# Kernel optimization log

Hardware: AMD Instinct MI355X
Metric: run time of the kernel (lower is better)

## Reference

```python
import jax, jax.numpy as jnp
import numpy as np

N_NODES = 200_000
BRANCH = 8      # n: one-hot width / max children encoded
K_DEPTH = 16    # k: number of stacked levels, h_emb = n*k


def setup_inputs() -> dict:
    b, N = BRANCH, N_NODES
    idx = np.arange(N, dtype=np.int64)
    # complete b-ary forest (single tree): parent of node i is (i-1)//b
    parent = np.maximum((idx - 1) // b, 0)
    child_idx = np.where(idx > 0, (idx - 1) % b, 0)
    # depth via level start offsets of a complete b-ary tree
    starts = np.array([(b ** d - 1) // (b - 1) for d in range(K_DEPTH + 1)], dtype=np.int64)
    depth = (np.searchsorted(starts, idx, side='right') - 1).astype(np.int32)
    # p_emb buffer: p**i with p = 1.0 (unused by the original forward)
    p_emb = jnp.ones((BRANCH * K_DEPTH,), dtype=jnp.float32)
    return {
        'parent': jnp.asarray(parent, jnp.int32),
        'child_idx': jnp.asarray(child_idx, jnp.int32),
        'depth': jnp.asarray(depth, jnp.int32),
        'p_emb': p_emb,
        'n': BRANCH,
        'k': K_DEPTH,
    }


def reference(parent, child_idx, depth, p_emb, n, k):
    """Level-parallel tree positional embedding.

    Original per-node loop: child.pos[n:] = parent.pos[:-n]; child.pos[:n] = eye_row.
    Equivalent top-down level sweep: at level d, every node takes its parent's
    embedding shifted right by n slots and prepends the one-hot of its sibling
    index (one_hot yields zeros for child_idx >= n, matching torch.eye rows).
    """
    N = parent.shape[0]
    h = n * k
    onehot = jax.nn.one_hot(child_idx, n, dtype=jnp.float32)  # [N, n]

    def body(d, emb):
        par = emb[parent]                                      # [N, h] gather
        shifted = jnp.concatenate([onehot, par[:, : h - n]], axis=1)
        return jnp.where((depth == d)[:, None], shifted, emb)

    emb0 = jnp.zeros((N, h), dtype=jnp.float32)                # roots stay zero
    pos_embeds = jax.lax.fori_loop(1, k + 1, body, emb0)
    return pos_embeds
```

## Files before the change

### kernel.cpp

```cpp
#include <hip/hip_runtime.h>


#define PE_K 16
#define ROWS_PER_BLOCK 128

typedef float vf4 __attribute__((ext_vector_type(4)));

__global__ __launch_bounds__(256) void PositionalEmbedding_kernel(
    const int* __restrict__ parent,
    const int* __restrict__ child_idx,
    const int* __restrict__ depth,
    float* __restrict__ out,
    int N) {
  __shared__ unsigned long long codes[ROWS_PER_BLOCK];

  const int tid  = threadIdx.x;
  const int row0 = blockIdx.x * ROWS_PER_BLOCK;

  if (tid < ROWS_PER_BLOCK) {
    int row = row0 + tid;
    unsigned long long code = 0;
    if (row < N) {
      int d  = depth[row];
      int dd = d < PE_K ? d : PE_K;
      int cur = row;
      for (int j = 0; j < dd; ++j) {
        int ci = child_idx[cur] & 7;
        code |= (unsigned long long)ci << (3 * j);
        cur = parent[cur];
      }
      code |= (unsigned long long)dd << 48;
    }
    codes[tid] = code;
  }
  __syncthreads();

  const int c  = tid & 31;
  const int g  = tid >> 5;
  const int j  = c >> 1;
  const int sh = 3 * j;
  const int r0 = 4 * c - 8 * j;

  vf4* p = reinterpret_cast<vf4*>(out) + ((long long)(row0 + g) * 32 + c);
  const int last_full_rl = N - row0;

  #pragma unroll
  for (int it = 0; it < ROWS_PER_BLOCK / 8; ++it) {
    int rl = it * 8 + g;
    unsigned long long code = codes[rl];
    int dd = (int)(code >> 48);
    int ci = (int)((code >> sh) & 7);
    ci = (j < dd) ? ci : 8;

    vf4 v;
    v.x = (ci == r0 + 0) ? 1.f : 0.f;
    v.y = (ci == r0 + 1) ? 1.f : 0.f;
    v.z = (ci == r0 + 2) ? 1.f : 0.f;
    v.w = (ci == r0 + 3) ? 1.f : 0.f;

    if (rl < last_full_rl) __builtin_nontemporal_store(v, p);
    p += 8 * 32;
  }
}

extern "C" void kernel_launch(void* const* d_in, const int* in_sizes, int n_in,
                              void* d_out, int out_size, void* d_ws, size_t ws_size,
                              hipStream_t stream) {
  const int* parent    = (const int*)d_in[0];
  const int* child_idx = (const int*)d_in[1];
  const int* depth     = (const int*)d_in[2];
  float* out = (float*)d_out;
  int N = in_sizes[0];

  int grid = (N + ROWS_PER_BLOCK - 1) / ROWS_PER_BLOCK;
  PositionalEmbedding_kernel<<<grid, 256, 0, stream>>>(parent, child_idx, depth, out, N);
}
```

Before: 25.78 us.

## Split tree walk and one-hot expansion into two kernels via workspace

Splits the fused kernel in two. The first kernel walks each node's ancestor chain and packs the sibling indices into 4-bit nibbles, writing one 64-bit code per node to the workspace; 8 is the sentinel for an empty slot. The second kernel expands these codes into the output with one float4 per thread across the whole grid, which removes the 128-row serial walk at block granularity and the shared-memory barrier. This adds a second launch and an extra global round-trip for the codes. It also replaces nontemporal stores with plain stores in the expand path and in the fallback fused kernel.

```diff
diff --git a/kernel.cpp b/kernel.cpp
--- a/kernel.cpp
+++ b/kernel.cpp
@@ -2,21 +2,62 @@
 
 
 #define PE_K 16
-#define ROWS_PER_BLOCK 128
 
 typedef float vf4 __attribute__((ext_vector_type(4)));
 
-__global__ __launch_bounds__(256) void PositionalEmbedding_kernel(
+__global__ __launch_bounds__(256) void pe_walk_kernel(
+    const int* __restrict__ parent,
+    const int* __restrict__ child_idx,
+    const int* __restrict__ depth,
+    unsigned long long* __restrict__ codes,
+    int N) {
+  int row = blockIdx.x * 256 + threadIdx.x;
+  if (row >= N) return;
+  unsigned long long code = 0x8888888888888888ULL;
+  int d  = depth[row];
+  int dd = d < PE_K ? d : PE_K;
+  int cur = row;
+  for (int j = 0; j < dd; ++j) {
+    unsigned long long ci = (unsigned long long)(child_idx[cur] & 7);
+    code = (code & ~(0xFULL << (4 * j))) | (ci << (4 * j));
+    cur = parent[cur];
+  }
+  codes[row] = code;
+}
+
+__global__ __launch_bounds__(256) void pe_expand_kernel(
+    const unsigned long long* __restrict__ codes,
+    float* __restrict__ out,
+    long long total_chunks) {
+  long long gid = (long long)blockIdx.x * 256 + threadIdx.x;
+  if (gid >= total_chunks) return;
+  int c = (int)(gid & 31);
+  long long row = gid >> 5;
+  int j  = c >> 1;
+  int r0 = 4 * c - 8 * j;
+
+  unsigned long long code = codes[row];
+  int ci = (int)((code >> (4 * j)) & 15);
+
+  vf4 v;
+  v.x = (ci == r0 + 0) ? 1.f : 0.f;
+  v.y = (ci == r0 + 1) ? 1.f : 0.f;
+  v.z = (ci == r0 + 2) ? 1.f : 0.f;
+  v.w = (ci == r0 + 3) ? 1.f : 0.f;
+
+  reinterpret_cast<vf4*>(out)[gid] = v;
+}
+
+#define ROWS_PER_BLOCK 128
+__global__ __launch_bounds__(256) void pe_fused_kernel(
     const int* __restrict__ parent,
     const int* __restrict__ child_idx,
     const int* __restrict__ depth,
     float* __restrict__ out,
     int N) {
   __shared__ unsigned long long codes[ROWS_PER_BLOCK];
-
   const int tid  = threadIdx.x;
   const int row0 = blockIdx.x * ROWS_PER_BLOCK;
-
   if (tid < ROWS_PER_BLOCK) {
     int row = row0 + tid;
     unsigned long long code = 0;
@@ -34,16 +75,13 @@
     codes[tid] = code;
   }
   __syncthreads();
-
   const int c  = tid & 31;
   const int g  = tid >> 5;
   const int j  = c >> 1;
   const int sh = 3 * j;
   const int r0 = 4 * c - 8 * j;
-
   vf4* p = reinterpret_cast<vf4*>(out) + ((long long)(row0 + g) * 32 + c);
   const int last_full_rl = N - row0;
-
   #pragma unroll
   for (int it = 0; it < ROWS_PER_BLOCK / 8; ++it) {
     int rl = it * 8 + g;
@@ -51,14 +89,12 @@
     int dd = (int)(code >> 48);
     int ci = (int)((code >> sh) & 7);
     ci = (j < dd) ? ci : 8;
-
     vf4 v;
     v.x = (ci == r0 + 0) ? 1.f : 0.f;
     v.y = (ci == r0 + 1) ? 1.f : 0.f;
     v.z = (ci == r0 + 2) ? 1.f : 0.f;
     v.w = (ci == r0 + 3) ? 1.f : 0.f;
-
-    if (rl < last_full_rl) __builtin_nontemporal_store(v, p);
+    if (rl < last_full_rl) *p = v;
     p += 8 * 32;
   }
 }
@@ -72,6 +108,15 @@
   float* out = (float*)d_out;
   int N = in_sizes[0];
 
-  int grid = (N + ROWS_PER_BLOCK - 1) / ROWS_PER_BLOCK;
-  PositionalEmbedding_kernel<<<grid, 256, 0, stream>>>(parent, child_idx, depth, out, N);
+  if (ws_size >= (size_t)N * 8) {
+    unsigned long long* codes = (unsigned long long*)d_ws;
+    int gridA = (N + 255) / 256;
+    pe_walk_kernel<<<gridA, 256, 0, stream>>>(parent, child_idx, depth, codes, N);
+    long long total_chunks = (long long)N * 32;
+    int gridB = (int)((total_chunks + 255) / 256);
+    pe_expand_kernel<<<gridB, 256, 0, stream>>>(codes, out, total_chunks);
+  } else {
+    int grid = (N + ROWS_PER_BLOCK - 1) / ROWS_PER_BLOCK;
+    pe_fused_kernel<<<grid, 256, 0, stream>>>(parent, child_idx, depth, out, N);
+  }
 }
```

Result: slower. 27.03 us (+4.9%).
